# Optimization experiments

Hardware: AMD Instinct MI355X
Metric: run time of the kernel (lower is better)

The kernel has to match this reference:

```python
import jax, jax.numpy as jnp
import numpy as np

B, S, D = 4, 1024, 1024
H = 16
HD = D // H  # head_dim = 64


def setup_inputs() -> dict:
    key = jax.random.key(0)
    k1, k2, k3 = jax.random.split(key, 3)
    x = jax.random.normal(k1, (B, S, D), dtype=jnp.float32)
    # qkv_proj: Linear(input_dim, 3*embed_dim), stored as (in, out) for x @ W
    scale = 1.0 / np.sqrt(D)
    W_qkv = jax.random.uniform(k2, (D, 3 * D), dtype=jnp.float32, minval=-scale, maxval=scale)
    b_qkv = jax.random.uniform(k3, (3 * D,), dtype=jnp.float32, minval=-scale, maxval=scale)
    return {"x": x, "W_qkv": W_qkv, "b_qkv": b_qkv}


def reference(x, W_qkv, b_qkv):
    b, s, _ = x.shape
    qkv = x @ W_qkv + b_qkv                       # [B,S,3D]
    qkv = qkv.reshape(b, s, H, 3 * HD)            # [B,S,H,3*hd]
    qkv = qkv.transpose(0, 2, 1, 3)               # [B,H,S,3*hd]
    q, k, v = jnp.split(qkv, 3, axis=-1)          # each [B,H,S,hd]
    scores = jnp.einsum('bhqd,bhkd->bhqk', q, k) / jnp.sqrt(jnp.float32(HD))
    attn = jax.nn.softmax(scores, axis=-1)        # [B,H,S,S]
    out = jnp.einsum('bhqk,bhkd->bhqd', attn, v)  # [B,H,S,hd]
    values = out.transpose(0, 2, 1, 3).reshape(b, s, H * HD)  # [B,S,D]
    return values
```

## Files before the change

kernel.cpp:

```cpp
#include <hip/hip_runtime.h>
#include <hip/hip_bf16.h>
#include <stdint.h>

#define BATCH 4
#define SEQ 1024
#define DMODEL 1024
#define NH 16
#define HD 64

typedef __attribute__((ext_vector_type(8))) short short8;
typedef __attribute__((ext_vector_type(4))) float f32x4;
typedef __attribute__((ext_vector_type(4))) unsigned short ushort4v;

__device__ __forceinline__ unsigned short f2bf(float f) {
    union { float f; uint32_t u; } v; v.f = f;
    uint32_t r = v.u + 0x7fff + ((v.u >> 16) & 1);
    return (unsigned short)(r >> 16);
}

__device__ __forceinline__ uint32_t pack2bf(float lo, float hi) {
    union { __hip_bfloat162 h; uint32_t u; } cv;
    cv.h = __float22bfloat162_rn(make_float2(lo, hi));
    return cv.u;
}

__global__ __launch_bounds__(256) void prep_kernel(const float* __restrict__ x,
                                                   const float* __restrict__ W,
                                                   unsigned short* __restrict__ xb,
                                                   unsigned short* __restrict__ Wt) {
    __shared__ float tile[32][33];
    int bid = blockIdx.x;
    if (bid < 2048) {
        int t = bid * 256 + threadIdx.x;
        const float4* p = (const float4*)x + (size_t)t * 2;
        float4 a = p[0], b = p[1];
        short8 o;
        o[0] = (short)f2bf(a.x); o[1] = (short)f2bf(a.y);
        o[2] = (short)f2bf(a.z); o[3] = (short)f2bf(a.w);
        o[4] = (short)f2bf(b.x); o[5] = (short)f2bf(b.y);
        o[6] = (short)f2bf(b.z); o[7] = (short)f2bf(b.w);
        *((short8*)xb + t) = o;
    } else {
        int r = bid - 2048;
        int nb = (r % 96) * 32;
        int kb = (r / 96) * 32;
        int tx = threadIdx.x & 31;
        int ty = threadIdx.x >> 5;
#pragma unroll
        for (int i = 0; i < 4; i++) {
            int k = kb + ty + i * 8;
            tile[ty + i * 8][tx] = W[(size_t)k * 3072 + nb + tx];
        }
        __syncthreads();
#pragma unroll
        for (int i = 0; i < 4; i++) {
            int n = nb + ty + i * 8;
            Wt[(size_t)n * 1024 + kb + tx] = f2bf(tile[tx][ty + i * 8]);
        }
    }
}

#define BM 128
#define BN 128
#define BKK 64
#define QSCALE 0.18033688011112042f

__global__ __launch_bounds__(256, 3) void qkv_gemm_kernel(
    const unsigned short* __restrict__ xb,
    const unsigned short* __restrict__ wt,
    const float* __restrict__ bias,
    unsigned short* __restrict__ Qb,
    unsigned short* __restrict__ Kb,
    unsigned short* __restrict__ VbT)
{
    __shared__ __align__(16) unsigned short As[BM][64];
    __shared__ __align__(16) unsigned short Bs[BN][64];
    int tid = threadIdx.x;
    int wave = tid >> 6, lane = tid & 63;
    int quad = lane >> 4, l16 = lane & 15;
    int wm = wave >> 1, wn = wave & 1;
    int m0 = blockIdx.x * BM;
    int n0 = blockIdx.y * BN;

    int grow = lane >> 3;
    int gcol = ((lane & 7) ^ grow) << 3;
    const unsigned short* gA = xb + (size_t)(m0 + wave * 32 + grow) * 1024 + gcol;
    const unsigned short* gB = wt + (size_t)(n0 + wave * 32 + grow) * 1024 + gcol;
    unsigned short* ldsA = &As[wave * 32][0] + lane * 8;
    unsigned short* ldsB = &Bs[wave * 32][0] + lane * 8;
    int sw = l16 & 7;

    short8 areg[4], breg[4];
#pragma unroll
    for (int i = 0; i < 4; i++) {
        areg[i] = *(const short8*)(gA + (size_t)i * 8 * 1024);
        breg[i] = *(const short8*)(gB + (size_t)i * 8 * 1024);
    }

    f32x4 acc[4][4] = {};
    for (int k0 = 0; k0 < 1024; k0 += BKK) {
        __syncthreads();
#pragma unroll
        for (int i = 0; i < 4; i++) {
            *(short8*)(ldsA + i * 512) = areg[i];
            *(short8*)(ldsB + i * 512) = breg[i];
        }
        __syncthreads();
        if (k0 + BKK < 1024) {
#pragma unroll
            for (int i = 0; i < 4; i++) {
                areg[i] = *(const short8*)(gA + (size_t)i * 8 * 1024 + k0 + BKK);
                breg[i] = *(const short8*)(gB + (size_t)i * 8 * 1024 + k0 + BKK);
            }
        }
#pragma unroll
        for (int kk = 0; kk < BKK; kk += 32) {
            int kb = kk >> 3;
            short8 af[4], bf[4];
#pragma unroll
            for (int t = 0; t < 4; t++) {
                int ar = wm * 64 + t * 16 + l16;
                af[t] = *(const short8*)&As[ar][((kb + quad) ^ sw) << 3];
            }
#pragma unroll
            for (int t = 0; t < 4; t++) {
                int br = wn * 64 + t * 16 + l16;
                bf[t] = *(const short8*)&Bs[br][((kb + quad) ^ sw) << 3];
            }
#pragma unroll
            for (int mt = 0; mt < 4; mt++)
#pragma unroll
                for (int nt = 0; nt < 4; nt++)
                    acc[mt][nt] = __builtin_amdgcn_mfma_f32_16x16x32_bf16(
                        af[mt], bf[nt], acc[mt][nt], 0, 0, 0);
        }
    }
#pragma unroll
    for (int nt = 0; nt < 4; nt++) {
        int n = n0 + wn * 64 + nt * 16 + l16;
        int h = n / 192;
        int c = n - h * 192;
        int which = c >> 6;
        int d = c & 63;
        float bv = bias[n];
        if (which == 2) {
#pragma unroll
            for (int mt = 0; mt < 4; mt++) {
                int m = m0 + wm * 64 + mt * 16 + quad * 4;
                int b = m >> 10, s = m & 1023;
                ushort4v o;
                o[0] = f2bf(acc[mt][nt][0] + bv);
                o[1] = f2bf(acc[mt][nt][1] + bv);
                o[2] = f2bf(acc[mt][nt][2] + bv);
                o[3] = f2bf(acc[mt][nt][3] + bv);
                *(ushort4v*)&VbT[((size_t)((b * 16 + h) * 64 + d)) * 1024 + s] = o;
            }
        } else {
            unsigned short* dst = (which == 0) ? Qb : Kb;
            float sc = (which == 0) ? QSCALE : 1.0f;
#pragma unroll
            for (int mt = 0; mt < 4; mt++) {
#pragma unroll
                for (int r = 0; r < 4; r++) {
                    int m = m0 + wm * 64 + mt * 16 + quad * 4 + r;
                    int b = m >> 10, s = m & 1023;
                    dst[((size_t)((b * 16 + h) * 1024 + s)) * 64 + d] = f2bf((acc[mt][nt][r] + bv) * sc);
                }
            }
        }
    }
}

#define BQ 64
#define BKV 128

__global__ __launch_bounds__(256, 2) void attn_kernel(
    const unsigned short* __restrict__ Qb,
    const unsigned short* __restrict__ Kb,
    const unsigned short* __restrict__ VbT,
    float* __restrict__ out)
{
    __shared__ __align__(16) char smem[32768];
    __shared__ float lbuf[4][4][16];
    unsigned short (*Ks)[64]  = (unsigned short(*)[64])smem;
    unsigned short (*Vts)[128] = (unsigned short(*)[128])(smem + 16384);
    float* red = (float*)smem;

    int tid = threadIdx.x;
    int wave = tid >> 6, lane = tid & 63;
    int quad = lane >> 4, l16 = lane & 15;

    int id = blockIdx.x;
    int xcd = id & 7, rest = id >> 3;
    int qt = rest & 15, grp = rest >> 4;
    int bh = grp * 8 + xcd;
    int q0 = qt * BQ;

    const unsigned short* Qp = Qb + (size_t)bh * SEQ * HD;
    const unsigned short* Kp = Kb + (size_t)bh * SEQ * HD;
    const unsigned short* Vp = VbT + (size_t)bh * HD * SEQ;

    int f_k = (l16 & 3) | (((l16 >> 2) & 1) << 2);
    int f_v = l16 & 7;
    int krow0 = (wave << 5) + ((l16 >> 2) << 3) + (l16 & 3);

    short8 qf[4][2];
#pragma unroll
    for (int g = 0; g < 4; g++)
#pragma unroll
        for (int kc = 0; kc < 2; kc++)
            qf[g][kc] = *(const short8*)&Qp[(size_t)(q0 + g * 16 + l16) * HD + kc * 32 + quad * 8];

    f32x4 oacc[4][4] = {};
    float lsum[4] = {0.f, 0.f, 0.f, 0.f};

    for (int kt = 0; kt < SEQ; kt += BKV) {
        __syncthreads();
#pragma unroll
        for (int i = 0; i < 4; i++) {
            int idx = i * 256 + tid;
            int krow = idx >> 3, kpb = idx & 7;
            int klb = kpb ^ ((krow & 3) | (((krow >> 3) & 1) << 2));
            *(short8*)&Ks[krow][kpb * 8] = *(const short8*)&Kp[(size_t)(kt + krow) * HD + klb * 8];
            int vrow = idx >> 4, vpb = idx & 15;
            int vlb = vpb ^ (vrow & 7);
            *(short8*)&Vts[vrow][vpb * 8] = *(const short8*)&Vp[(size_t)vrow * SEQ + kt + vlb * 8];
        }
        __syncthreads();

        short8 kf[2][2], vf[4];
#pragma unroll
        for (int t = 0; t < 2; t++)
#pragma unroll
            for (int kc = 0; kc < 2; kc++)
                kf[t][kc] = *(const short8*)&Ks[krow0 + t * 4][(((kc << 2) + quad) ^ f_k) * 8];
#pragma unroll
        for (int nt = 0; nt < 4; nt++)
            vf[nt] = *(const short8*)&Vts[nt * 16 + l16][(((wave << 2) + quad) ^ f_v) * 8];

#pragma unroll
        for (int g = 0; g < 4; g++) {
            f32x4 s0 = {}, s1 = {};
#pragma unroll
            for (int kc = 0; kc < 2; kc++) {
                s0 = __builtin_amdgcn_mfma_f32_16x16x32_bf16(kf[0][kc], qf[g][kc], s0, 0, 0, 0);
                s1 = __builtin_amdgcn_mfma_f32_16x16x32_bf16(kf[1][kc], qf[g][kc], s1, 0, 0, 0);
            }
            float p0 = __builtin_amdgcn_exp2f(s0[0]);
            float p1 = __builtin_amdgcn_exp2f(s0[1]);
            float p2 = __builtin_amdgcn_exp2f(s0[2]);
            float p3 = __builtin_amdgcn_exp2f(s0[3]);
            float p4 = __builtin_amdgcn_exp2f(s1[0]);
            float p5 = __builtin_amdgcn_exp2f(s1[1]);
            float p6 = __builtin_amdgcn_exp2f(s1[2]);
            float p7 = __builtin_amdgcn_exp2f(s1[3]);
            lsum[g] += ((p0 + p1) + (p2 + p3)) + ((p4 + p5) + (p6 + p7));
            union { uint32_t w[4]; short8 s; } pf;
            pf.w[0] = pack2bf(p0, p1);
            pf.w[1] = pack2bf(p2, p3);
            pf.w[2] = pack2bf(p4, p5);
            pf.w[3] = pack2bf(p6, p7);
#pragma unroll
            for (int nt = 0; nt < 4; nt++)
                oacc[g][nt] = __builtin_amdgcn_mfma_f32_16x16x32_bf16(vf[nt], pf.s, oacc[g][nt], 0, 0, 0);
        }
    }

#pragma unroll
    for (int g = 0; g < 4; g++) {
        lsum[g] += __shfl_xor(lsum[g], 16, 64);
        lsum[g] += __shfl_xor(lsum[g], 32, 64);
    }
    int off = quad * 16 + l16;
    __syncthreads();
    if (wave >= 2) {
        float* r = red + (wave - 2) * 4096;
#pragma unroll
        for (int g = 0; g < 4; g++)
#pragma unroll
            for (int nt = 0; nt < 4; nt++)
#pragma unroll
                for (int rr = 0; rr < 4; rr++)
                    r[((g * 4 + nt) * 4 + rr) * 64 + off] = oacc[g][nt][rr];
        if (quad == 0)
#pragma unroll
            for (int g = 0; g < 4; g++) lbuf[wave][g][l16] = lsum[g];
    }
    __syncthreads();
    if (wave < 2) {
        float* r = red + wave * 4096;
#pragma unroll
        for (int g = 0; g < 4; g++) {
#pragma unroll
            for (int nt = 0; nt < 4; nt++)
#pragma unroll
                for (int rr = 0; rr < 4; rr++)
                    oacc[g][nt][rr] += r[((g * 4 + nt) * 4 + rr) * 64 + off];
            lsum[g] += lbuf[wave + 2][g][l16];
        }
    }
    __syncthreads();
    if (wave == 1) {
#pragma unroll
        for (int g = 0; g < 4; g++)
#pragma unroll
            for (int nt = 0; nt < 4; nt++)
#pragma unroll
                for (int rr = 0; rr < 4; rr++)
                    red[((g * 4 + nt) * 4 + rr) * 64 + off] = oacc[g][nt][rr];
        if (quad == 0)
#pragma unroll
            for (int g = 0; g < 4; g++) lbuf[1][g][l16] = lsum[g];
    }
    __syncthreads();
    if (wave == 0) {
        int b = bh >> 4, h = bh & 15;
#pragma unroll
        for (int g = 0; g < 4; g++) {
            float l = lsum[g] + lbuf[1][g][l16];
            float inv = 1.f / l;
            int s = q0 + g * 16 + l16;
#pragma unroll
            for (int nt = 0; nt < 4; nt++) {
                float4 o;
                o.x = (oacc[g][nt][0] + red[((g * 4 + nt) * 4 + 0) * 64 + off]) * inv;
                o.y = (oacc[g][nt][1] + red[((g * 4 + nt) * 4 + 1) * 64 + off]) * inv;
                o.z = (oacc[g][nt][2] + red[((g * 4 + nt) * 4 + 2) * 64 + off]) * inv;
                o.w = (oacc[g][nt][3] + red[((g * 4 + nt) * 4 + 3) * 64 + off]) * inv;
                *(float4*)&out[(size_t)(b * SEQ + s) * DMODEL + h * HD + nt * 16 + quad * 4] = o;
            }
        }
    }
}

extern "C" void kernel_launch(void* const* d_in, const int* in_sizes, int n_in,
                              void* d_out, int out_size, void* d_ws, size_t ws_size,
                              hipStream_t stream) {
    const float* x    = (const float*)d_in[0];
    const float* W    = (const float*)d_in[1];
    const float* bias = (const float*)d_in[2];
    float* out = (float*)d_out;
    char* ws = (char*)d_ws;

    unsigned short* xb  = (unsigned short*)(ws);
    unsigned short* wt  = (unsigned short*)(ws + 8388608);
    unsigned short* Qb  = (unsigned short*)(ws + 14680064);
    unsigned short* Kb  = (unsigned short*)(ws + 23068672);
    unsigned short* VbT = (unsigned short*)(ws + 31457280);

    prep_kernel<<<5120, 256, 0, stream>>>(x, W, xb, wt);
    dim3 gg(32, 24);
    qkv_gemm_kernel<<<gg, 256, 0, stream>>>(xb, wt, bias, Qb, Kb, VbT);
    attn_kernel<<<1024, 256, 0, stream>>>(Qb, Kb, VbT, out);
}
```

Baseline: 145.4 us.

## Double attention query tile to 128 with 2x2 wave split; XCD-aware GEMM block mapping

The attention kernel now handles 128 queries per block. Waves split as two query halves times two key halves, so each K/V tile loaded into LDS serves twice as many queries, and the cross-wave reduction drops from a two-stage tree to a single exchange. The QKV GEMM grid becomes 1D with a swizzled mapping that groups M/N tiles per XCD to improve L2 reuse. The attention launch halves to 512 blocks, which may lower occupancy and load balance across CUs.

```diff
diff --git a/kernel.cpp b/kernel.cpp
--- a/kernel.cpp
+++ b/kernel.cpp
@@ -79,8 +79,13 @@
     int wave = tid >> 6, lane = tid & 63;
     int quad = lane >> 4, l16 = lane & 15;
     int wm = wave >> 1, wn = wave & 1;
-    int m0 = blockIdx.x * BM;
-    int n0 = blockIdx.y * BN;
+
+    int id = blockIdx.x;
+    int x = id & 7, r = id >> 3;
+    int m_t = (x & 3) * 8 + (r & 7);
+    int n_t = (x >> 2) * 12 + (r >> 3);
+    int m0 = m_t * BM;
+    int n0 = n_t * BN;
 
     int grow = lane >> 3;
     int gcol = ((lane & 7) ^ grow) << 3;
@@ -161,17 +166,17 @@
 #pragma unroll
             for (int mt = 0; mt < 4; mt++) {
 #pragma unroll
-                for (int r = 0; r < 4; r++) {
-                    int m = m0 + wm * 64 + mt * 16 + quad * 4 + r;
+                for (int r2 = 0; r2 < 4; r2++) {
+                    int m = m0 + wm * 64 + mt * 16 + quad * 4 + r2;
                     int b = m >> 10, s = m & 1023;
-                    dst[((size_t)((b * 16 + h) * 1024 + s)) * 64 + d] = f2bf((acc[mt][nt][r] + bv) * sc);
+                    dst[((size_t)((b * 16 + h) * 1024 + s)) * 64 + d] = f2bf((acc[mt][nt][r2] + bv) * sc);
                 }
             }
         }
     }
 }
 
-#define BQ 64
+#define BQ 128
 #define BKV 128
 
 __global__ __launch_bounds__(256, 2) void attn_kernel(
@@ -182,17 +187,18 @@
 {
     __shared__ __align__(16) char smem[32768];
     __shared__ float lbuf[4][4][16];
-    unsigned short (*Ks)[64]  = (unsigned short(*)[64])smem;
+    unsigned short (*Ks)[64]   = (unsigned short(*)[64])smem;
     unsigned short (*Vts)[128] = (unsigned short(*)[128])(smem + 16384);
     float* red = (float*)smem;
 
     int tid = threadIdx.x;
     int wave = tid >> 6, lane = tid & 63;
     int quad = lane >> 4, l16 = lane & 15;
+    int qh = wave & 1, kh = wave >> 1;
 
     int id = blockIdx.x;
     int xcd = id & 7, rest = id >> 3;
-    int qt = rest & 15, grp = rest >> 4;
+    int qt = rest & 7, grp = rest >> 3;
     int bh = grp * 8 + xcd;
     int q0 = qt * BQ;
 
@@ -202,14 +208,14 @@
 
     int f_k = (l16 & 3) | (((l16 >> 2) & 1) << 2);
     int f_v = l16 & 7;
-    int krow0 = (wave << 5) + ((l16 >> 2) << 3) + (l16 & 3);
+    int prow = (kh << 6) + ((l16 >> 2) << 3) + (l16 & 3);
 
     short8 qf[4][2];
 #pragma unroll
     for (int g = 0; g < 4; g++)
 #pragma unroll
         for (int kc = 0; kc < 2; kc++)
-            qf[g][kc] = *(const short8*)&Qp[(size_t)(q0 + g * 16 + l16) * HD + kc * 32 + quad * 8];
+            qf[g][kc] = *(const short8*)&Qp[(size_t)(q0 + qh * 64 + g * 16 + l16) * HD + kc * 32 + quad * 8];
 
     f32x4 oacc[4][4] = {};
     float lsum[4] = {0.f, 0.f, 0.f, 0.f};
@@ -228,41 +234,45 @@
         }
         __syncthreads();
 
-        short8 kf[2][2], vf[4];
-#pragma unroll
-        for (int t = 0; t < 2; t++)
-#pragma unroll
-            for (int kc = 0; kc < 2; kc++)
-                kf[t][kc] = *(const short8*)&Ks[krow0 + t * 4][(((kc << 2) + quad) ^ f_k) * 8];
-#pragma unroll
-        for (int nt = 0; nt < 4; nt++)
-            vf[nt] = *(const short8*)&Vts[nt * 16 + l16][(((wave << 2) + quad) ^ f_v) * 8];
-
-#pragma unroll
-        for (int g = 0; g < 4; g++) {
-            f32x4 s0 = {}, s1 = {};
+#pragma unroll
+        for (int c = 0; c < 2; c++) {
+            int base = prow + (c << 5);
+            short8 kf0[2], kf1[2];
 #pragma unroll
             for (int kc = 0; kc < 2; kc++) {
-                s0 = __builtin_amdgcn_mfma_f32_16x16x32_bf16(kf[0][kc], qf[g][kc], s0, 0, 0, 0);
-                s1 = __builtin_amdgcn_mfma_f32_16x16x32_bf16(kf[1][kc], qf[g][kc], s1, 0, 0, 0);
-            }
-            float p0 = __builtin_amdgcn_exp2f(s0[0]);
-            float p1 = __builtin_amdgcn_exp2f(s0[1]);
-            float p2 = __builtin_amdgcn_exp2f(s0[2]);
-            float p3 = __builtin_amdgcn_exp2f(s0[3]);
-            float p4 = __builtin_amdgcn_exp2f(s1[0]);
-            float p5 = __builtin_amdgcn_exp2f(s1[1]);
-            float p6 = __builtin_amdgcn_exp2f(s1[2]);
-            float p7 = __builtin_amdgcn_exp2f(s1[3]);
-            lsum[g] += ((p0 + p1) + (p2 + p3)) + ((p4 + p5) + (p6 + p7));
-            union { uint32_t w[4]; short8 s; } pf;
-            pf.w[0] = pack2bf(p0, p1);
-            pf.w[1] = pack2bf(p2, p3);
-            pf.w[2] = pack2bf(p4, p5);
-            pf.w[3] = pack2bf(p6, p7);
+                kf0[kc] = *(const short8*)&Ks[base][(((kc << 2) + quad) ^ f_k) * 8];
+                kf1[kc] = *(const short8*)&Ks[base + 4][(((kc << 2) + quad) ^ f_k) * 8];
+            }
+            short8 vf[4];
 #pragma unroll
             for (int nt = 0; nt < 4; nt++)
-                oacc[g][nt] = __builtin_amdgcn_mfma_f32_16x16x32_bf16(vf[nt], pf.s, oacc[g][nt], 0, 0, 0);
+                vf[nt] = *(const short8*)&Vts[nt * 16 + l16][(((kh << 3) + (c << 2) + quad) ^ f_v) * 8];
+#pragma unroll
+            for (int g = 0; g < 4; g++) {
+                f32x4 s0 = {}, s1 = {};
+#pragma unroll
+                for (int kc = 0; kc < 2; kc++) {
+                    s0 = __builtin_amdgcn_mfma_f32_16x16x32_bf16(kf0[kc], qf[g][kc], s0, 0, 0, 0);
+                    s1 = __builtin_amdgcn_mfma_f32_16x16x32_bf16(kf1[kc], qf[g][kc], s1, 0, 0, 0);
+                }
+                float p0 = __builtin_amdgcn_exp2f(s0[0]);
+                float p1 = __builtin_amdgcn_exp2f(s0[1]);
+                float p2 = __builtin_amdgcn_exp2f(s0[2]);
+                float p3 = __builtin_amdgcn_exp2f(s0[3]);
+                float p4 = __builtin_amdgcn_exp2f(s1[0]);
+                float p5 = __builtin_amdgcn_exp2f(s1[1]);
+                float p6 = __builtin_amdgcn_exp2f(s1[2]);
+                float p7 = __builtin_amdgcn_exp2f(s1[3]);
+                lsum[g] += ((p0 + p1) + (p2 + p3)) + ((p4 + p5) + (p6 + p7));
+                union { uint32_t w[4]; short8 s; } pf;
+                pf.w[0] = pack2bf(p0, p1);
+                pf.w[1] = pack2bf(p2, p3);
+                pf.w[2] = pack2bf(p4, p5);
+                pf.w[3] = pack2bf(p6, p7);
+#pragma unroll
+                for (int nt = 0; nt < 4; nt++)
+                    oacc[g][nt] = __builtin_amdgcn_mfma_f32_16x16x32_bf16(vf[nt], pf.s, oacc[g][nt], 0, 0, 0);
+            }
         }
     }
 
@@ -273,60 +283,35 @@
     }
     int off = quad * 16 + l16;
     __syncthreads();
-    if (wave >= 2) {
-        float* r = red + (wave - 2) * 4096;
+    if (kh == 1) {
+        float* rp = red + qh * 4096;
 #pragma unroll
         for (int g = 0; g < 4; g++)
 #pragma unroll
             for (int nt = 0; nt < 4; nt++)
 #pragma unroll
                 for (int rr = 0; rr < 4; rr++)
-                    r[((g * 4 + nt) * 4 + rr) * 64 + off] = oacc[g][nt][rr];
+                    rp[((g * 4 + nt) * 4 + rr) * 64 + off] = oacc[g][nt][rr];
         if (quad == 0)
 #pragma unroll
             for (int g = 0; g < 4; g++) lbuf[wave][g][l16] = lsum[g];
     }
     __syncthreads();
-    if (wave < 2) {
-        float* r = red + wave * 4096;
+    if (kh == 0) {
+        float* rp = red + qh * 4096;
+        int b = bh >> 4, h = bh & 15;
 #pragma unroll
         for (int g = 0; g < 4; g++) {
-#pragma unroll
-            for (int nt = 0; nt < 4; nt++)
-#pragma unroll
-                for (int rr = 0; rr < 4; rr++)
-                    oacc[g][nt][rr] += r[((g * 4 + nt) * 4 + rr) * 64 + off];
-            lsum[g] += lbuf[wave + 2][g][l16];
-        }
-    }
-    __syncthreads();
-    if (wave == 1) {
-#pragma unroll
-        for (int g = 0; g < 4; g++)
-#pragma unroll
-            for (int nt = 0; nt < 4; nt++)
-#pragma unroll
-                for (int rr = 0; rr < 4; rr++)
-                    red[((g * 4 + nt) * 4 + rr) * 64 + off] = oacc[g][nt][rr];
-        if (quad == 0)
-#pragma unroll
-            for (int g = 0; g < 4; g++) lbuf[1][g][l16] = lsum[g];
-    }
-    __syncthreads();
-    if (wave == 0) {
-        int b = bh >> 4, h = bh & 15;
-#pragma unroll
-        for (int g = 0; g < 4; g++) {
-            float l = lsum[g] + lbuf[1][g][l16];
+            float l = lsum[g] + lbuf[wave + 2][g][l16];
             float inv = 1.f / l;
-            int s = q0 + g * 16 + l16;
+            int s = q0 + qh * 64 + g * 16 + l16;
 #pragma unroll
             for (int nt = 0; nt < 4; nt++) {
                 float4 o;
-                o.x = (oacc[g][nt][0] + red[((g * 4 + nt) * 4 + 0) * 64 + off]) * inv;
-                o.y = (oacc[g][nt][1] + red[((g * 4 + nt) * 4 + 1) * 64 + off]) * inv;
-                o.z = (oacc[g][nt][2] + red[((g * 4 + nt) * 4 + 2) * 64 + off]) * inv;
-                o.w = (oacc[g][nt][3] + red[((g * 4 + nt) * 4 + 3) * 64 + off]) * inv;
+                o.x = (oacc[g][nt][0] + rp[((g * 4 + nt) * 4 + 0) * 64 + off]) * inv;
+                o.y = (oacc[g][nt][1] + rp[((g * 4 + nt) * 4 + 1) * 64 + off]) * inv;
+                o.z = (oacc[g][nt][2] + rp[((g * 4 + nt) * 4 + 2) * 64 + off]) * inv;
+                o.w = (oacc[g][nt][3] + rp[((g * 4 + nt) * 4 + 3) * 64 + off]) * inv;
                 *(float4*)&out[(size_t)(b * SEQ + s) * DMODEL + h * HD + nt * 16 + quad * 4] = o;
             }
         }
@@ -349,7 +334,6 @@
     unsigned short* VbT = (unsigned short*)(ws + 31457280);
 
     prep_kernel<<<5120, 256, 0, stream>>>(x, W, xb, wt);
-    dim3 gg(32, 24);
-    qkv_gemm_kernel<<<gg, 256, 0, stream>>>(xb, wt, bias, Qb, Kb, VbT);
-    attn_kernel<<<1024, 256, 0, stream>>>(Qb, Kb, VbT, out);
-}
+    qkv_gemm_kernel<<<768, 256, 0, stream>>>(xb, wt, bias, Qb, Kb, VbT);
+    attn_kernel<<<512, 256, 0, stream>>>(Qb, Kb, VbT, out);
+}
```

Measured after the change: 137.6 us. 1.06x faster.
